# Kernel tuning notes

Hardware: AMD Instinct MI355X
Metric: run time of the kernel (lower is better)

Reference implementation:

```python
import jax, jax.numpy as jnp
import numpy as np
from jax import lax

B, N, C_IN, C_OUT = 4, 8192, 64, 128
STRIDE, RADIUS, K, L = 4, 0.1, 32, 2
EPS = 1e-5
M = N // STRIDE


def _bn(x, g, b):
    # training-mode batch norm, channel-first layout (B, C, ...)
    axes = (0,) + tuple(range(2, x.ndim))
    mean = jnp.mean(x, axis=axes, keepdims=True)
    var = jnp.mean((x - mean) ** 2, axis=axes, keepdims=True)
    sh = (1, -1) + (1,) * (x.ndim - 2)
    return (x - mean) * lax.rsqrt(var + EPS) * g.reshape(sh) + b.reshape(sh)


def _fps(points, m):
    # farthest point sampling starting at index 0 (matches fps_cuda semantics)
    b, n, _ = points.shape
    bi = jnp.arange(b)

    def body(carry, _):
        dis, last = carry
        lp = points[bi, last]  # (b,3)
        d = jnp.sum((points - lp[:, None, :]) ** 2, -1)
        dis = jnp.minimum(dis, d)
        return (dis, jnp.argmax(dis, -1).astype(jnp.int32)), last

    init = (jnp.full((b, n), 1e10, points.dtype), jnp.zeros((b,), jnp.int32))
    _, idx = lax.scan(body, init, None, length=m)
    return idx.T  # (b, m)


def _ball_query(radius, k, centroids, points, features):
    # first k points within radius of each centroid; pad with first hit
    b, n, _ = points.shape
    d2 = jnp.sum((centroids[:, :, None, :] - points[:, None, :, :]) ** 2, -1)  # (b,m,n)
    key = jnp.where(d2 < radius * radius, jnp.arange(n, dtype=jnp.int32), n)
    neg, _ = lax.top_k(-key, k)  # k smallest keys = first k in-ball indices
    sel = -neg  # (b,m,k)
    sel = jnp.where(sel == n, sel[..., :1], sel)
    sel = jnp.clip(sel, 0, n - 1)
    bi = jnp.arange(b)[:, None, None]
    gp = jnp.transpose(points[bi, sel], (0, 3, 2, 1))  # (b,3,k,m)
    gf = None
    if features is not None:
        gf = jnp.transpose(features[bi, sel], (0, 3, 2, 1))  # (b,c,k,m)
    return gp, gf


def _forward(pos, x, p):
    b, n, _ = pos.shape
    m = n // STRIDE
    bi = jnp.arange(b)[:, None]
    fps_idx = _fps(pos, m)
    centroids = pos[bi, fps_idx]  # (b,m,3)
    # x_mlp: 1x1 conv + BN + ReLU
    f = jax.nn.relu(_bn(jnp.einsum('bnc,oc->bon', x, p['W_x']), p['g_x'], p['b_x']))
    feats = jnp.transpose(f, (0, 2, 1))  # (b,n,C_OUT)
    gp, gf = _ball_query(RADIUS, K, centroids, pos, feats)
    cT = jnp.transpose(centroids, (0, 2, 1))[:, :, None, :]  # (b,3,1,m)
    gp = (gp - cT) / RADIUS
    gp = jax.nn.relu(_bn(jnp.einsum('bckm,oc->bokm', gp, p['W_ps']), p['g_ps'], p['b_ps']))
    xf = jnp.transpose(jnp.max(gf + gp, axis=2), (0, 2, 1))  # (b,m,C_OUT)
    # gen_pe on downsampled points
    R2 = RADIUS * 2
    gpe, _ = _ball_query(R2, K, centroids, centroids, None)
    gpe = (gpe - cT) / R2
    pe = jax.nn.relu(_bn(jnp.einsum('bckm,oc->bokm', gpe, p['W_pe']), p['g_pe'], p['b_pe']))
    # InvResMLP blocks
    for i in range(L):
        xc = jnp.transpose(xf, (0, 2, 1))  # (b,C,m)
        xc = jax.nn.relu(_bn(jnp.einsum('bcm,oc->bom', xc, p['W1'][i]), p['g1'][i], p['b1'][i]))
        feats_i = jnp.transpose(xc, (0, 2, 1))  # (b,m,C)
        _, gfi = _ball_query(R2, K, centroids, centroids, feats_i)
        g = jnp.max(gfi + pe, axis=2)  # (b,C,m)
        g = jax.nn.relu(_bn(jnp.einsum('bcm,oc->bom', g, p['W2a'][i]), p['g2a'][i], p['b2a'][i]))
        g = _bn(jnp.einsum('bcm,oc->bom', g, p['W2b'][i]), p['g2b'][i], p['b2b'][i])
        xf = jax.nn.relu(feats_i + jnp.transpose(g, (0, 2, 1)))
    return centroids, xf


def setup_inputs() -> dict:
    key = jax.random.key(0)
    ks = jax.random.split(key, 12)
    d = {
        'pos': jax.random.uniform(ks[0], (B, N, 3), jnp.float32),
        'x': jax.random.normal(ks[1], (B, N, C_IN), jnp.float32),
        'W_x': jax.random.normal(ks[2], (C_OUT, C_IN), jnp.float32) * 0.05,
        'g_x': jnp.ones((C_OUT,), jnp.float32), 'b_x': jnp.zeros((C_OUT,), jnp.float32),
        'W_ps': jax.random.normal(ks[3], (C_OUT, 3), jnp.float32) * 0.1,
        'g_ps': jnp.ones((C_OUT,), jnp.float32), 'b_ps': jnp.zeros((C_OUT,), jnp.float32),
        'W_pe': jax.random.normal(ks[4], (C_OUT, 3), jnp.float32) * 0.1,
        'g_pe': jnp.ones((C_OUT,), jnp.float32), 'b_pe': jnp.zeros((C_OUT,), jnp.float32),
        'W1': jax.random.normal(ks[5], (L, C_OUT, C_OUT), jnp.float32) * 0.05,
        'g1': jnp.ones((L, C_OUT), jnp.float32), 'b1': jnp.zeros((L, C_OUT), jnp.float32),
        'W2a': jax.random.normal(ks[6], (L, C_OUT, C_OUT), jnp.float32) * 0.05,
        'g2a': jnp.ones((L, C_OUT), jnp.float32), 'b2a': jnp.zeros((L, C_OUT), jnp.float32),
        'W2b': jax.random.normal(ks[7], (L, C_OUT, C_OUT), jnp.float32) * 0.05,
        'g2b': jnp.ones((L, C_OUT), jnp.float32), 'b2b': jnp.zeros((L, C_OUT), jnp.float32),
    }
    return d


def reference(pos, x, W_x, g_x, b_x, W_ps, g_ps, b_ps, W_pe, g_pe, b_pe,
              W1, g1, b1, W2a, g2a, b2a, W2b, g2b, b2b):
    p = dict(W_x=W_x, g_x=g_x, b_x=b_x, W_ps=W_ps, g_ps=g_ps, b_ps=b_ps,
             W_pe=W_pe, g_pe=g_pe, b_pe=b_pe, W1=W1, g1=g1, b1=b1,
             W2a=W2a, g2a=g2a, b2a=b2a, W2b=W2b, g2b=g2b, b2b=b2b)
    return _forward(pos, x, p)
```

## Files before the change

kernel.cpp:

```cpp
#include <hip/hip_runtime.h>


#define BB 4
#define NN 8192
#define MM 2048
#define KK 32
#define CI 64
#define CO 128
#define SG 16

typedef float vf2 __attribute__((ext_vector_type(2)));

#define ST_X 0
#define MO_PS 256
#define MO_PE 272
#define ST1 288
#define ST2A 800
#define ST2B (800 + 2 * SG * 256)
#define ST_TOTAL (ST2B + 512)

__device__ __forceinline__ float sq3(float dx, float dy, float dz) {
#pragma clang fp contract(off)
  return dx * dx + dy * dy + dz * dz;
}

__device__ __forceinline__ void fin_stats_d(const double* st, float gam,
                                            float bet, double cnt, int ch,
                                            float* sc, float* sh) {
  double mean = st[ch] / cnt;
  double var = st[128 + ch] / cnt - mean * mean;
  if (var < 0) var = 0;
  double s = (double)gam / sqrt(var + 1e-5);
  *sc = (float)s;
  *sh = (float)((double)bet - mean * s);
}

__device__ __forceinline__ void fin_mom_d(const double* mo, const float* Wrow,
                                          float gam, float bet, double cnt,
                                          float* sc, float* sh) {
  double w0 = Wrow[0], w1 = Wrow[1], w2 = Wrow[2];
  double mx = mo[0] / cnt, my = mo[1] / cnt, mz = mo[2] / cnt;
  double sxx = mo[3] / cnt, sxy = mo[4] / cnt, sxz = mo[5] / cnt;
  double syy = mo[6] / cnt, syz = mo[7] / cnt, szz = mo[8] / cnt;
  double mean = w0 * mx + w1 * my + w2 * mz;
  double ey2 = w0 * w0 * sxx + w1 * w1 * syy + w2 * w2 * szz +
               2.0 * (w0 * w1 * sxy + w0 * w2 * sxz + w1 * w2 * syz);
  double var = ey2 - mean * mean;
  if (var < 0) var = 0;
  double s = (double)gam / sqrt(var + 1e-5);
  *sc = (float)s;
  *sh = (float)((double)bet - mean * s);
}

__global__ void k_zero(double* s) {
  int i = blockIdx.x * 256 + threadIdx.x;
  if (i < ST_TOTAL) s[i] = 0.0;
}

template <int CTRL>
__device__ __forceinline__ int dpp_i(int v) {
  return __builtin_amdgcn_update_dpp(v, v, CTRL, 0xF, 0xF, false);
}
template <int CTRL>
__device__ __forceinline__ float dpp_f(float v) {
  return __int_as_float(dpp_i<CTRL>(__float_as_int(v)));
}

#define FT 512
#define NP 8
#define NW 8

__global__ __launch_bounds__(FT) void k_fps_conv(
    const float* __restrict__ pos, const float* __restrict__ x,
    const float* __restrict__ W_x, float* __restrict__ cent,
    float* __restrict__ fpre, double* __restrict__ stats) {
  __shared__ alignas(16) float s_wv[NW];
  __shared__ alignas(16) int s_wi[NW];
  __shared__ alignas(16) float s_pts[NN * 3];
  int t = threadIdx.x;
  if (blockIdx.x >= BB) {
    int cb = blockIdx.x - BB;
    int o = t & 127, q = t >> 7;
    float4 w[CI / 4];
    const float4* Wv = (const float4*)(W_x + (size_t)o * CI);
#pragma unroll
    for (int i = 0; i < CI / 4; i++) w[i] = Wv[i];
    int row0 = cb * 128;
    float ssum = 0.f, ssq = 0.f;
    for (int r = 0; r < 128; r += 4) {
      int row = __builtin_amdgcn_readfirstlane(row0 + r + q);
      const float* xr = x + (size_t)row * CI;
      float acc = 0.f;
#pragma unroll
      for (int i = 0; i < CI / 4; i++) {
        float4 a = *(const float4*)(xr + 4 * i);
        acc += a.x * w[i].x + a.y * w[i].y + a.z * w[i].z + a.w * w[i].w;
      }
      fpre[(size_t)row * CO + o] = acc;
      ssum += acc;
      ssq += acc * acc;
    }
    atomicAdd(&stats[ST_X + o], (double)ssum);
    atomicAdd(&stats[ST_X + 128 + o], (double)ssq);
    return;
  }
  int b = blockIdx.x;
  const float* P = pos + (size_t)b * NN * 3;
  float* C = cent + (size_t)b * MM * 3;
  int lane = t & 63, w = t >> 6;
  for (int i = t; i < (NN * 3) / 4; i += FT) {
    ((float4*)s_pts)[i] = ((const float4*)P)[i];
  }
  vf2 px[NP], py[NP], pz[NP], ds[NP];
#pragma unroll
  for (int s = 0; s < NP; s++) {
    int ia = (2 * s) * FT + t;
    int ib = ia + FT;
    px[s] = (vf2){P[ia * 3 + 0], P[ib * 3 + 0]};
    py[s] = (vf2){P[ia * 3 + 1], P[ib * 3 + 1]};
    pz[s] = (vf2){P[ia * 3 + 2], P[ib * 3 + 2]};
    ds[s] = (vf2){1e10f, 1e10f};
  }
  float lx = P[0], ly = P[1], lz = P[2];
  if (t == 0) {
    C[0] = lx;
    C[1] = ly;
    C[2] = lz;
  }
  __syncthreads();
  for (int m = 1; m < MM; m++) {
    vf2 l2x = (vf2){lx, lx}, l2y = (vf2){ly, ly}, l2z = (vf2){lz, lz};
    vf2 bmax = (vf2){-1.0f, -1.0f};
    {
#pragma clang fp contract(off)
#pragma unroll
      for (int s = 0; s < NP; s++) {
        vf2 dx = px[s] - l2x;
        vf2 dy = py[s] - l2y;
        vf2 dz = pz[s] - l2z;
        vf2 d2 = dx * dx + dy * dy + dz * dz;
        vf2 nd = __builtin_elementwise_min(ds[s], d2);
        ds[s] = nd;
        bmax = __builtin_elementwise_max(bmax, nd);
      }
    }
    float bv = fmaxf(bmax.x, bmax.y);
    bv = fmaxf(bv, dpp_f<0x111>(bv));
    bv = fmaxf(bv, dpp_f<0x112>(bv));
    bv = fmaxf(bv, dpp_f<0x114>(bv));
    bv = fmaxf(bv, dpp_f<0x118>(bv));
    bv = fmaxf(bv, dpp_f<0x142>(bv));
    bv = fmaxf(bv, dpp_f<0x143>(bv));
    if (lane == 63) s_wv[w] = bv;
    float gw63 =
        __int_as_float(__builtin_amdgcn_readlane(__float_as_int(bv), 63));
    __syncthreads();
    float4 va = ((const float4*)s_wv)[0];
    float4 vb = ((const float4*)s_wv)[1];
    float gmax = fmaxf(fmaxf(fmaxf(va.x, va.y), fmaxf(va.z, va.w)),
                       fmaxf(fmaxf(vb.x, vb.y), fmaxf(vb.z, vb.w)));
    int bi = 0x7fffffff;
    if (gw63 == gmax) {
#pragma unroll
      for (int s = 0; s < NP; s++) {
        int ia = (2 * s) * FT + t;
        int ib2 = ia + FT;
        bi = (ds[s].x == gmax) ? (ia < bi ? ia : bi) : bi;
        bi = (ds[s].y == gmax) ? (ib2 < bi ? ib2 : bi) : bi;
      }
      int u;
      u = dpp_i<0x111>(bi); bi = u < bi ? u : bi;
      u = dpp_i<0x112>(bi); bi = u < bi ? u : bi;
      u = dpp_i<0x114>(bi); bi = u < bi ? u : bi;
      u = dpp_i<0x118>(bi); bi = u < bi ? u : bi;
      u = dpp_i<0x142>(bi); bi = u < bi ? u : bi;
      u = dpp_i<0x143>(bi); bi = u < bi ? u : bi;
    }
    if (lane == 63) s_wi[w] = bi;
    __syncthreads();
    int4 ia4 = ((const int4*)s_wi)[0];
    int4 ib4 = ((const int4*)s_wi)[1];
    int g0 = ia4.x < ia4.y ? ia4.x : ia4.y;
    int g1 = ia4.z < ia4.w ? ia4.z : ia4.w;
    int g2 = ib4.x < ib4.y ? ib4.x : ib4.y;
    int g3 = ib4.z < ib4.w ? ib4.z : ib4.w;
    g0 = g0 < g1 ? g0 : g1;
    g2 = g2 < g3 ? g2 : g3;
    int gidx = g0 < g2 ? g0 : g2;
    lx = s_pts[gidx * 3 + 0];
    ly = s_pts[gidx * 3 + 1];
    lz = s_pts[gidx * 3 + 2];
    if (t == 0) {
      C[m * 3 + 0] = lx;
      C[m * 3 + 1] = ly;
      C[m * 3 + 2] = lz;
    }
  }
}

__global__ __launch_bounds__(256) void k_bq2(const float* __restrict__ pos,
                                             const float* __restrict__ cent,
                                             int* __restrict__ sel1,
                                             int* __restrict__ sel2,
                                             double* __restrict__ stats) {
  int lane = threadIdx.x & 63, w = threadIdx.x >> 6;
  const float* pts;
  int npts, pair;
  float rsq, inv_r;
  int* sel;
  double* mom;
  int half = (BB * MM) / 4;
  if (blockIdx.x < half) {
    pts = pos; npts = NN; rsq = 0.01f; inv_r = 10.0f;
    sel = sel1; mom = stats + MO_PS;
    pair = blockIdx.x * 4 + w;
  } else {
    pts = cent; npts = MM; rsq = 0.04f; inv_r = 5.0f;
    sel = sel2; mom = stats + MO_PE;
    pair = (blockIdx.x - half) * 4 + w;
  }
  int b = pair / MM;
  const float* P = pts + (size_t)b * npts * 3;
  const float* C = cent + (size_t)pair * 3;
  float cx = C[0], cy = C[1], cz = C[2];
  __shared__ int s_sel[4][KK];
  __shared__ float s_mom[4][9];
  int cnt = 0;
  int nch = npts >> 6;
  for (int ch = 0; ch < nch; ch++) {
    int i = (ch << 6) + lane;
    float d2 = sq3(P[i * 3 + 0] - cx, P[i * 3 + 1] - cy, P[i * 3 + 2] - cz);
    bool hit = d2 < rsq;
    unsigned long long mk = __ballot(hit);
    if (mk) {
      int pre = __popcll(mk & ((1ull << lane) - 1ull));
      int k = cnt + pre;
      if (hit && k < KK) s_sel[w][k] = i;
      cnt += __popcll(mk);
      if (cnt >= KK) break;
    }
  }
  int total = cnt < KK ? cnt : KK;
  int myidx = 0;
  if (lane < KK) {
    int v = (lane < total) ? s_sel[w][lane] : s_sel[w][0];
    sel[(size_t)pair * KK + lane] = v;
    myidx = v;
  }
  float gx = 0.f, gy = 0.f, gz = 0.f;
  if (lane < KK) {
    gx = (P[myidx * 3 + 0] - cx) * inv_r;
    gy = (P[myidx * 3 + 1] - cy) * inv_r;
    gz = (P[myidx * 3 + 2] - cz) * inv_r;
  }
  float v9[9] = {gx, gy, gz, gx * gx, gx * gy, gx * gz, gy * gy, gy * gz, gz * gz};
#pragma unroll
  for (int j = 0; j < 9; j++) {
#pragma unroll
    for (int off = 32; off > 0; off >>= 1) v9[j] += __shfl_xor(v9[j], off);
  }
  if (lane == 0) {
#pragma unroll
    for (int j = 0; j < 9; j++) s_mom[w][j] = v9[j];
  }
  __syncthreads();
  if (threadIdx.x < 9) {
    double a = (double)s_mom[0][threadIdx.x] + s_mom[1][threadIdx.x] +
               s_mom[2][threadIdx.x] + s_mom[3][threadIdx.x];
    atomicAdd(&mom[threadIdx.x], a);
  }
}

__global__ __launch_bounds__(128) void k_xf(
    const float* __restrict__ pos, const float* __restrict__ cent,
    const int* __restrict__ sel1, const float* __restrict__ fpre,
    const float* __restrict__ Wps, const float* __restrict__ g_ps,
    const float* __restrict__ b_ps, const float* __restrict__ g_x,
    const float* __restrict__ b_x, const double* __restrict__ stats,
    float* __restrict__ xf) {
  int pair = blockIdx.x;
  int b = pair >> 11;
  int o = threadIdx.x;
  float sx, hx, sp, hp;
  fin_stats_d(stats + ST_X, g_x[o], b_x[o], (double)(BB * NN), o, &sx, &hx);
  fin_mom_d(stats + MO_PS, Wps + o * 3, g_ps[o], b_ps[o],
            (double)(BB * MM * KK), &sp, &hp);
  float w0 = Wps[o * 3 + 0], w1 = Wps[o * 3 + 1], w2 = Wps[o * 3 + 2];
  const float* C = cent + (size_t)pair * 3;
  float cx = C[0], cy = C[1], cz = C[2];
  const float* P = pos + (size_t)b * NN * 3;
  const float* F = fpre + (size_t)b * NN * CO;
  __shared__ int s_idx[KK];
  if (o < KK) s_idx[o] = sel1[(size_t)pair * KK + o];
  __syncthreads();
  float acc = -1e30f;
#pragma unroll 4
  for (int k = 0; k < KK; k++) {
    int idx = __builtin_amdgcn_readfirstlane(s_idx[k]);
    float gx = (P[idx * 3 + 0] - cx) * 10.0f;
    float gy = (P[idx * 3 + 1] - cy) * 10.0f;
    float gz = (P[idx * 3 + 2] - cz) * 10.0f;
    float y = fmaxf((w0 * gx + w1 * gy + w2 * gz) * sp + hp, 0.f);
    float f = fmaxf(F[(size_t)idx * CO + o] * sx + hx, 0.f);
    float v = y + f;
    acc = v > acc ? v : acc;
  }
  xf[(size_t)pair * CO + o] = acc;
}

__global__ __launch_bounds__(256) void k_conv_plain(
    const float* __restrict__ in, const float* __restrict__ W,
    float* __restrict__ out, double* __restrict__ stats, int rows_per_block) {
  int o = threadIdx.x & 127, half = threadIdx.x >> 7;
  float4 w[CO / 4];
  const float4* Wv = (const float4*)(W + (size_t)o * CO);
#pragma unroll
  for (int i = 0; i < CO / 4; i++) w[i] = Wv[i];
  int row0 = blockIdx.x * rows_per_block;
  float ssum = 0.f, ssq = 0.f;
  for (int r = 0; r < rows_per_block; r += 2) {
    int row = __builtin_amdgcn_readfirstlane(row0 + r + half);
    const float* xr = in + (size_t)row * CO;
    float acc = 0.f;
#pragma unroll
    for (int i = 0; i < CO / 4; i++) {
      float4 a = *(const float4*)(xr + 4 * i);
      acc += a.x * w[i].x + a.y * w[i].y + a.z * w[i].z + a.w * w[i].w;
    }
    out[(size_t)row * CO + o] = acc;
    ssum += acc;
    ssq += acc * acc;
  }
  atomicAdd(&stats[o], (double)ssum);
  atomicAdd(&stats[128 + o], (double)ssq);
}

__global__ __launch_bounds__(256) void k_conv_bnin(
    const float* __restrict__ in, const float* __restrict__ W,
    const double* __restrict__ st_grp, const float* __restrict__ gam,
    const float* __restrict__ bet, float* __restrict__ out,
    double* __restrict__ stats, int rows_per_block) {
  __shared__ float s_sc[128], s_sh[128];
  int t = threadIdx.x;
  if (t < 128) {
    double sum = 0, ssq2 = 0;
#pragma unroll
    for (int g = 0; g < SG; g++) {
      sum += st_grp[g * 256 + t];
      ssq2 += st_grp[g * 256 + 128 + t];
    }
    double cnt = (double)(BB * MM);
    double mean = sum / cnt;
    double var = ssq2 / cnt - mean * mean;
    if (var < 0) var = 0;
    double s = (double)gam[t] / sqrt(var + 1e-5);
    s_sc[t] = (float)s;
    s_sh[t] = (float)((double)bet[t] - mean * s);
  }
  __syncthreads();
  int o = t & 127, half = t >> 7;
  float4 w[CO / 4];
  const float4* Wv = (const float4*)(W + (size_t)o * CO);
#pragma unroll
  for (int i = 0; i < CO / 4; i++) w[i] = Wv[i];
  int row0 = blockIdx.x * rows_per_block;
  float ssum = 0.f, ssq = 0.f;
  for (int r = 0; r < rows_per_block; r += 2) {
    int row = __builtin_amdgcn_readfirstlane(row0 + r + half);
    const float* xr = in + (size_t)row * CO;
    float acc = 0.f;
#pragma unroll
    for (int i = 0; i < CO / 4; i++) {
      float4 a = *(const float4*)(xr + 4 * i);
      a.x = fmaxf(a.x * s_sc[4 * i + 0] + s_sh[4 * i + 0], 0.f);
      a.y = fmaxf(a.y * s_sc[4 * i + 1] + s_sh[4 * i + 1], 0.f);
      a.z = fmaxf(a.z * s_sc[4 * i + 2] + s_sh[4 * i + 2], 0.f);
      a.w = fmaxf(a.w * s_sc[4 * i + 3] + s_sh[4 * i + 3], 0.f);
      acc += a.x * w[i].x + a.y * w[i].y + a.z * w[i].z + a.w * w[i].w;
    }
    out[(size_t)row * CO + o] = acc;
    ssum += acc;
    ssq += acc * acc;
  }
  atomicAdd(&stats[o], (double)ssum);
  atomicAdd(&stats[128 + o], (double)ssq);
}

__global__ __launch_bounds__(256) void k_conv_resid(
    const float* __restrict__ y1prev, const float* __restrict__ y2bprev,
    const double* __restrict__ st1p, const float* __restrict__ g1p,
    const float* __restrict__ b1p, const double* __restrict__ st2bp,
    const float* __restrict__ g2bp, const float* __restrict__ b2bp,
    const float* __restrict__ W, float* __restrict__ y1out,
    double* __restrict__ stats, int rows_per_block) {
  __shared__ float s_s1[128], s_h1[128], s_s2[128], s_h2[128];
  int t = threadIdx.x;
  if (t < 128) {
    fin_stats_d(st1p, g1p[t], b1p[t], (double)(BB * MM), t, &s_s1[t], &s_h1[t]);
    fin_stats_d(st2bp, g2bp[t], b2bp[t], (double)(BB * MM), t, &s_s2[t],
                &s_h2[t]);
  }
  __syncthreads();
  int o = t & 127, half = t >> 7;
  float4 w[CO / 4];
  const float4* Wv = (const float4*)(W + (size_t)o * CO);
#pragma unroll
  for (int i = 0; i < CO / 4; i++) w[i] = Wv[i];
  int row0 = blockIdx.x * rows_per_block;
  float ssum = 0.f, ssq = 0.f;
  for (int r = 0; r < rows_per_block; r += 2) {
    int row = __builtin_amdgcn_readfirstlane(row0 + r + half);
    const float* ar = y1prev + (size_t)row * CO;
    const float* br = y2bprev + (size_t)row * CO;
    float acc = 0.f;
#pragma unroll
    for (int i = 0; i < CO / 4; i++) {
      float4 a = *(const float4*)(ar + 4 * i);
      float4 bb = *(const float4*)(br + 4 * i);
      float x0 = fmaxf(fmaxf(a.x * s_s1[4 * i + 0] + s_h1[4 * i + 0], 0.f) +
                           (bb.x * s_s2[4 * i + 0] + s_h2[4 * i + 0]), 0.f);
      float x1 = fmaxf(fmaxf(a.y * s_s1[4 * i + 1] + s_h1[4 * i + 1], 0.f) +
                           (bb.y * s_s2[4 * i + 1] + s_h2[4 * i + 1]), 0.f);
      float x2 = fmaxf(fmaxf(a.z * s_s1[4 * i + 2] + s_h1[4 * i + 2], 0.f) +
                           (bb.z * s_s2[4 * i + 2] + s_h2[4 * i + 2]), 0.f);
      float x3 = fmaxf(fmaxf(a.w * s_s1[4 * i + 3] + s_h1[4 * i + 3], 0.f) +
                           (bb.w * s_s2[4 * i + 3] + s_h2[4 * i + 3]), 0.f);
      acc += x0 * w[i].x + x1 * w[i].y + x2 * w[i].z + x3 * w[i].w;
    }
    y1out[(size_t)row * CO + o] = acc;
    ssum += acc;
    ssq += acc * acc;
  }
  atomicAdd(&stats[o], (double)ssum);
  atomicAdd(&stats[128 + o], (double)ssq);
}

__global__ __launch_bounds__(128) void k_gconv(
    const float* __restrict__ cent, const int* __restrict__ sel2,
    const float* __restrict__ y1in, const double* __restrict__ st1,
    const float* __restrict__ g1v, const float* __restrict__ b1v,
    const double* __restrict__ mo_pe, const float* __restrict__ Wpe,
    const float* __restrict__ gpe, const float* __restrict__ bpe,
    const float* __restrict__ W2a, float* __restrict__ y2a,
    double* __restrict__ st2a) {
  int pair = blockIdx.x;
  int b = pair >> 11;
  int o = threadIdx.x;
  float s1, h1, se, he;
  fin_stats_d(st1, g1v[o], b1v[o], (double)(BB * MM), o, &s1, &h1);
  fin_mom_d(mo_pe, Wpe + o * 3, gpe[o], bpe[o], (double)(BB * MM * KK), &se,
            &he);
  float w0 = Wpe[o * 3 + 0], w1 = Wpe[o * 3 + 1], w2 = Wpe[o * 3 + 2];
  const float* C = cent + (size_t)pair * 3;
  float cx = C[0], cy = C[1], cz = C[2];
  const float* CB = cent + (size_t)b * MM * 3;
  const float* Y = y1in + (size_t)b * MM * CO;
  __shared__ int s_idx[KK];
  __shared__ float s_g[128];
  if (o < KK) s_idx[o] = sel2[(size_t)pair * KK + o];
  __syncthreads();
  float acc = -1e30f;
#pragma unroll 4
  for (int k = 0; k < KK; k++) {
    int idx = __builtin_amdgcn_readfirstlane(s_idx[k]);
    float gx = (CB[idx * 3 + 0] - cx) * 5.0f;
    float gy = (CB[idx * 3 + 1] - cy) * 5.0f;
    float gz = (CB[idx * 3 + 2] - cz) * 5.0f;
    float pe = fmaxf((w0 * gx + w1 * gy + w2 * gz) * se + he, 0.f);
    float f = fmaxf(Y[(size_t)idx * CO + o] * s1 + h1, 0.f);
    float v = pe + f;
    acc = v > acc ? v : acc;
  }
  s_g[o] = acc;
  __syncthreads();
  const float4* Wv = (const float4*)(W2a + (size_t)o * CO);
  const float4* gv = (const float4*)s_g;
  float dot = 0.f;
#pragma unroll
  for (int i = 0; i < CO / 4; i++) {
    float4 a = gv[i];
    float4 ww = Wv[i];
    dot += a.x * ww.x + a.y * ww.y + a.z * ww.z + a.w * ww.w;
  }
  y2a[(size_t)pair * CO + o] = dot;
  int grp = pair & (SG - 1);
  atomicAdd(&st2a[grp * 256 + o], (double)dot);
  atomicAdd(&st2a[grp * 256 + 128 + o], (double)(dot * dot));
}

__global__ __launch_bounds__(256) void k_resid_fin(
    const float* __restrict__ y1b, const double* __restrict__ st1,
    const float* __restrict__ g1v, const float* __restrict__ b1v,
    const float* __restrict__ y2b, const double* __restrict__ st2b,
    const float* __restrict__ g2bv, const float* __restrict__ b2bv,
    float* __restrict__ xf) {
  int i = blockIdx.x * 256 + threadIdx.x;
  int o = i & 127;
  float s1, h1, s2, h2;
  fin_stats_d(st1, g1v[o], b1v[o], (double)(BB * MM), o, &s1, &h1);
  fin_stats_d(st2b, g2bv[o], b2bv[o], (double)(BB * MM), o, &s2, &h2);
  float f = fmaxf(y1b[i] * s1 + h1, 0.f);
  float v = y2b[i] * s2 + h2;
  xf[i] = fmaxf(f + v, 0.f);
}

extern "C" void kernel_launch(void* const* d_in, const int* in_sizes, int n_in,
                              void* d_out, int out_size, void* d_ws,
                              size_t ws_size, hipStream_t stream) {
  const float* pos = (const float*)d_in[0];
  const float* x = (const float*)d_in[1];
  const float* W_x = (const float*)d_in[2];
  const float* g_x = (const float*)d_in[3];
  const float* b_x = (const float*)d_in[4];
  const float* W_ps = (const float*)d_in[5];
  const float* g_ps = (const float*)d_in[6];
  const float* b_ps = (const float*)d_in[7];
  const float* W_pe = (const float*)d_in[8];
  const float* g_pe = (const float*)d_in[9];
  const float* b_pe = (const float*)d_in[10];
  const float* W1 = (const float*)d_in[11];
  const float* g1 = (const float*)d_in[12];
  const float* b1 = (const float*)d_in[13];
  const float* W2a = (const float*)d_in[14];
  const float* g2a = (const float*)d_in[15];
  const float* b2a = (const float*)d_in[16];
  const float* W2b = (const float*)d_in[17];
  const float* g2b = (const float*)d_in[18];
  const float* b2b = (const float*)d_in[19];

  float* cent = (float*)d_out;
  float* xf = cent + (size_t)BB * MM * 3;

  char* p = (char*)d_ws;
  double* stats = (double*)p; p += (size_t)ST_TOTAL * sizeof(double);
  int* sel1 = (int*)p;        p += (size_t)BB * MM * KK * sizeof(int);
  int* sel2 = (int*)p;        p += (size_t)BB * MM * KK * sizeof(int);
  float* fpre = (float*)p;    p += (size_t)BB * NN * CO * sizeof(float);
  float* y1a = (float*)p;     p += (size_t)BB * MM * CO * sizeof(float);
  float* y1b = (float*)p;     p += (size_t)BB * MM * CO * sizeof(float);
  float* y2a = (float*)p;     p += (size_t)BB * MM * CO * sizeof(float);
  float* y2b = (float*)p;     p += (size_t)BB * MM * CO * sizeof(float);

  k_zero<<<(ST_TOTAL + 255) / 256, 256, 0, stream>>>(stats);
  k_fps_conv<<<BB + 256, FT, 0, stream>>>(pos, x, W_x, cent, fpre, stats);
  k_bq2<<<(BB * MM) / 2, 256, 0, stream>>>(pos, cent, sel1, sel2, stats);
  k_xf<<<BB * MM, 128, 0, stream>>>(pos, cent, sel1, fpre, W_ps, g_ps, b_ps,
                                    g_x, b_x, stats, xf);
  k_conv_plain<<<128, 256, 0, stream>>>(xf, W1, y1a, stats + ST1, 64);
  k_gconv<<<BB * MM, 128, 0, stream>>>(cent, sel2, y1a, stats + ST1, g1, b1,
                                       stats + MO_PE, W_pe, g_pe, b_pe, W2a,
                                       y2a, stats + ST2A);
  k_conv_bnin<<<128, 256, 0, stream>>>(y2a, W2b, stats + ST2A, g2a, b2a, y2b,
                                       stats + ST2B, 64);
  k_conv_resid<<<128, 256, 0, stream>>>(
      y1a, y2b, stats + ST1, g1, b1, stats + ST2B, g2b, b2b, W1 + CO * CO, y1b,
      stats + ST1 + 256, 64);
  k_gconv<<<BB * MM, 128, 0, stream>>>(cent, sel2, y1b, stats + ST1 + 256,
                                       g1 + 128, b1 + 128, stats + MO_PE, W_pe,
                                       g_pe, b_pe, W2a + CO * CO, y2a,
                                       stats + ST2A + SG * 256);
  k_conv_bnin<<<128, 256, 0, stream>>>(y2a, W2b + CO * CO,
                                       stats + ST2A + SG * 256, g2a + 128,
                                       b2a + 128, y2b, stats + ST2B + 256, 64);
  k_resid_fin<<<(BB * MM * CO) / 256, 256, 0, stream>>>(
      y1b, stats + ST1 + 256, g1 + 128, b1 + 128, y2b, stats + ST2B + 256,
      g2b + 128, b2b + 128, xf);
}
```

Baseline: 2.687 ms.

## Fuse neighbor max-pool with first conv, group BN stats, unroll ball query

The neighbor max-pool kernel now also computes the first 128x128 conv per centroid from shared memory, which removes the separate k_conv_plain launch and the xf round trip. Its per-channel BN statistics are spread across SG grouped slots to cut atomic contention, and consumers sum the groups through a new fin_grp_d helper. The ball-query scan handles four 64-point chunks per iteration to expose more memory-level parallelism, at the cost of possibly scanning past the early-exit point. The zeroing kernel is replaced by hipMemsetAsync. The fused kernel issues one double atomic pair per block per channel (8192 blocks), which may itself create atomic traffic.

```diff
diff --git a/kernel.cpp b/kernel.cpp
--- a/kernel.cpp
+++ b/kernel.cpp
@@ -15,8 +15,8 @@
 #define MO_PS 256
 #define MO_PE 272
 #define ST1 288
-#define ST2A 800
-#define ST2B (800 + 2 * SG * 256)
+#define ST2A (288 + 2 * SG * 256)
+#define ST2B (ST2A + 2 * SG * 256)
 #define ST_TOTAL (ST2B + 512)
 
 __device__ __forceinline__ float sq3(float dx, float dy, float dz) {
@@ -29,6 +29,23 @@
                                             float* sc, float* sh) {
   double mean = st[ch] / cnt;
   double var = st[128 + ch] / cnt - mean * mean;
+  if (var < 0) var = 0;
+  double s = (double)gam / sqrt(var + 1e-5);
+  *sc = (float)s;
+  *sh = (float)((double)bet - mean * s);
+}
+
+__device__ __forceinline__ void fin_grp_d(const double* st, float gam,
+                                          float bet, double cnt, int ch,
+                                          float* sc, float* sh) {
+  double sum = 0, ssq = 0;
+#pragma unroll
+  for (int g = 0; g < SG; g++) {
+    sum += st[g * 256 + ch];
+    ssq += st[g * 256 + 128 + ch];
+  }
+  double mean = sum / cnt;
+  double var = ssq / cnt - mean * mean;
   if (var < 0) var = 0;
   double s = (double)gam / sqrt(var + 1e-5);
   *sc = (float)s;
@@ -50,11 +67,6 @@
   double s = (double)gam / sqrt(var + 1e-5);
   *sc = (float)s;
   *sh = (float)((double)bet - mean * s);
-}
-
-__global__ void k_zero(double* s) {
-  int i = blockIdx.x * 256 + threadIdx.x;
-  if (i < ST_TOTAL) s[i] = 0.0;
 }
 
 template <int CTRL>
@@ -226,19 +238,49 @@
   __shared__ int s_sel[4][KK];
   __shared__ float s_mom[4][9];
   int cnt = 0;
-  int nch = npts >> 6;
-  for (int ch = 0; ch < nch; ch++) {
-    int i = (ch << 6) + lane;
-    float d2 = sq3(P[i * 3 + 0] - cx, P[i * 3 + 1] - cy, P[i * 3 + 2] - cz);
-    bool hit = d2 < rsq;
-    unsigned long long mk = __ballot(hit);
-    if (mk) {
-      int pre = __popcll(mk & ((1ull << lane) - 1ull));
-      int k = cnt + pre;
-      if (hit && k < KK) s_sel[w][k] = i;
-      cnt += __popcll(mk);
-      if (cnt >= KK) break;
-    }
+  unsigned long long ltm = (1ull << lane) - 1ull;
+  int nit = npts >> 8;
+  for (int ch = 0; ch < nit; ch++) {
+    int i0 = (ch << 8) + lane;
+    bool h0, h1, h2, h3;
+    {
+      float a0 = P[i0 * 3 + 0], a1 = P[i0 * 3 + 1], a2 = P[i0 * 3 + 2];
+      float b0 = P[(i0 + 64) * 3 + 0], b1 = P[(i0 + 64) * 3 + 1],
+            b2 = P[(i0 + 64) * 3 + 2];
+      float c0 = P[(i0 + 128) * 3 + 0], c1 = P[(i0 + 128) * 3 + 1],
+            c2 = P[(i0 + 128) * 3 + 2];
+      float e0 = P[(i0 + 192) * 3 + 0], e1 = P[(i0 + 192) * 3 + 1],
+            e2 = P[(i0 + 192) * 3 + 2];
+      h0 = sq3(a0 - cx, a1 - cy, a2 - cz) < rsq;
+      h1 = sq3(b0 - cx, b1 - cy, b2 - cz) < rsq;
+      h2 = sq3(c0 - cx, c1 - cy, c2 - cz) < rsq;
+      h3 = sq3(e0 - cx, e1 - cy, e2 - cz) < rsq;
+    }
+    unsigned long long m0 = __ballot(h0);
+    unsigned long long m1 = __ballot(h1);
+    unsigned long long m2 = __ballot(h2);
+    unsigned long long m3 = __ballot(h3);
+    if (m0) {
+      int k = cnt + __popcll(m0 & ltm);
+      if (h0 && k < KK) s_sel[w][k] = i0;
+      cnt += __popcll(m0);
+    }
+    if (m1) {
+      int k = cnt + __popcll(m1 & ltm);
+      if (h1 && k < KK) s_sel[w][k] = i0 + 64;
+      cnt += __popcll(m1);
+    }
+    if (m2) {
+      int k = cnt + __popcll(m2 & ltm);
+      if (h2 && k < KK) s_sel[w][k] = i0 + 128;
+      cnt += __popcll(m2);
+    }
+    if (m3) {
+      int k = cnt + __popcll(m3 & ltm);
+      if (h3 && k < KK) s_sel[w][k] = i0 + 192;
+      cnt += __popcll(m3);
+    }
+    if (cnt >= KK) break;
   }
   int total = cnt < KK ? cnt : KK;
   int myidx = 0;
@@ -271,13 +313,14 @@
   }
 }
 
-__global__ __launch_bounds__(128) void k_xf(
+__global__ __launch_bounds__(128) void k_xf_conv1(
     const float* __restrict__ pos, const float* __restrict__ cent,
     const int* __restrict__ sel1, const float* __restrict__ fpre,
     const float* __restrict__ Wps, const float* __restrict__ g_ps,
     const float* __restrict__ b_ps, const float* __restrict__ g_x,
     const float* __restrict__ b_x, const double* __restrict__ stats,
-    float* __restrict__ xf) {
+    const float* __restrict__ W1, float* __restrict__ y1a,
+    double* __restrict__ st1out) {
   int pair = blockIdx.x;
   int b = pair >> 11;
   int o = threadIdx.x;
@@ -291,6 +334,7 @@
   const float* P = pos + (size_t)b * NN * 3;
   const float* F = fpre + (size_t)b * NN * CO;
   __shared__ int s_idx[KK];
+  __shared__ float s_xf[128];
   if (o < KK) s_idx[o] = sel1[(size_t)pair * KK + o];
   __syncthreads();
   float acc = -1e30f;
@@ -305,34 +349,21 @@
     float v = y + f;
     acc = v > acc ? v : acc;
   }
-  xf[(size_t)pair * CO + o] = acc;
-}
-
-__global__ __launch_bounds__(256) void k_conv_plain(
-    const float* __restrict__ in, const float* __restrict__ W,
-    float* __restrict__ out, double* __restrict__ stats, int rows_per_block) {
-  int o = threadIdx.x & 127, half = threadIdx.x >> 7;
-  float4 w[CO / 4];
-  const float4* Wv = (const float4*)(W + (size_t)o * CO);
-#pragma unroll
-  for (int i = 0; i < CO / 4; i++) w[i] = Wv[i];
-  int row0 = blockIdx.x * rows_per_block;
-  float ssum = 0.f, ssq = 0.f;
-  for (int r = 0; r < rows_per_block; r += 2) {
-    int row = __builtin_amdgcn_readfirstlane(row0 + r + half);
-    const float* xr = in + (size_t)row * CO;
-    float acc = 0.f;
-#pragma unroll
-    for (int i = 0; i < CO / 4; i++) {
-      float4 a = *(const float4*)(xr + 4 * i);
-      acc += a.x * w[i].x + a.y * w[i].y + a.z * w[i].z + a.w * w[i].w;
-    }
-    out[(size_t)row * CO + o] = acc;
-    ssum += acc;
-    ssq += acc * acc;
-  }
-  atomicAdd(&stats[o], (double)ssum);
-  atomicAdd(&stats[128 + o], (double)ssq);
+  s_xf[o] = acc;
+  __syncthreads();
+  const float4* Wv = (const float4*)(W1 + (size_t)o * CO);
+  const float4* gv = (const float4*)s_xf;
+  float dot = 0.f;
+#pragma unroll
+  for (int i = 0; i < CO / 4; i++) {
+    float4 a = gv[i];
+    float4 ww = Wv[i];
+    dot += a.x * ww.x + a.y * ww.y + a.z * ww.z + a.w * ww.w;
+  }
+  y1a[(size_t)pair * CO + o] = dot;
+  int grp = pair & (SG - 1);
+  atomicAdd(&st1out[grp * 256 + o], (double)dot);
+  atomicAdd(&st1out[grp * 256 + 128 + o], (double)(dot * dot));
 }
 
 __global__ __launch_bounds__(256) void k_conv_bnin(
@@ -343,19 +374,8 @@
   __shared__ float s_sc[128], s_sh[128];
   int t = threadIdx.x;
   if (t < 128) {
-    double sum = 0, ssq2 = 0;
-#pragma unroll
-    for (int g = 0; g < SG; g++) {
-      sum += st_grp[g * 256 + t];
-      ssq2 += st_grp[g * 256 + 128 + t];
-    }
-    double cnt = (double)(BB * MM);
-    double mean = sum / cnt;
-    double var = ssq2 / cnt - mean * mean;
-    if (var < 0) var = 0;
-    double s = (double)gam[t] / sqrt(var + 1e-5);
-    s_sc[t] = (float)s;
-    s_sh[t] = (float)((double)bet[t] - mean * s);
+    fin_grp_d(st_grp, gam[t], bet[t], (double)(BB * MM), t, &s_sc[t],
+              &s_sh[t]);
   }
   __syncthreads();
   int o = t & 127, half = t >> 7;
@@ -396,7 +416,7 @@
   __shared__ float s_s1[128], s_h1[128], s_s2[128], s_h2[128];
   int t = threadIdx.x;
   if (t < 128) {
-    fin_stats_d(st1p, g1p[t], b1p[t], (double)(BB * MM), t, &s_s1[t], &s_h1[t]);
+    fin_grp_d(st1p, g1p[t], b1p[t], (double)(BB * MM), t, &s_s1[t], &s_h1[t]);
     fin_stats_d(st2bp, g2bp[t], b2bp[t], (double)(BB * MM), t, &s_s2[t],
                 &s_h2[t]);
   }
@@ -431,8 +451,9 @@
     ssum += acc;
     ssq += acc * acc;
   }
-  atomicAdd(&stats[o], (double)ssum);
-  atomicAdd(&stats[128 + o], (double)ssq);
+  int grp = blockIdx.x & (SG - 1);
+  atomicAdd(&stats[grp * 256 + o], (double)ssum);
+  atomicAdd(&stats[grp * 256 + 128 + o], (double)ssq);
 }
 
 __global__ __launch_bounds__(128) void k_gconv(
@@ -447,7 +468,7 @@
   int b = pair >> 11;
   int o = threadIdx.x;
   float s1, h1, se, he;
-  fin_stats_d(st1, g1v[o], b1v[o], (double)(BB * MM), o, &s1, &h1);
+  fin_grp_d(st1, g1v[o], b1v[o], (double)(BB * MM), o, &s1, &h1);
   fin_mom_d(mo_pe, Wpe + o * 3, gpe[o], bpe[o], (double)(BB * MM * KK), &se,
             &he);
   float w0 = Wpe[o * 3 + 0], w1 = Wpe[o * 3 + 1], w2 = Wpe[o * 3 + 2];
@@ -497,7 +518,7 @@
   int i = blockIdx.x * 256 + threadIdx.x;
   int o = i & 127;
   float s1, h1, s2, h2;
-  fin_stats_d(st1, g1v[o], b1v[o], (double)(BB * MM), o, &s1, &h1);
+  fin_grp_d(st1, g1v[o], b1v[o], (double)(BB * MM), o, &s1, &h1);
   fin_stats_d(st2b, g2bv[o], b2bv[o], (double)(BB * MM), o, &s2, &h2);
   float f = fmaxf(y1b[i] * s1 + h1, 0.f);
   float v = y2b[i] * s2 + h2;
@@ -541,12 +562,12 @@
   float* y2a = (float*)p;     p += (size_t)BB * MM * CO * sizeof(float);
   float* y2b = (float*)p;     p += (size_t)BB * MM * CO * sizeof(float);
 
-  k_zero<<<(ST_TOTAL + 255) / 256, 256, 0, stream>>>(stats);
+  hipMemsetAsync(stats, 0, (size_t)ST_TOTAL * sizeof(double), stream);
   k_fps_conv<<<BB + 256, FT, 0, stream>>>(pos, x, W_x, cent, fpre, stats);
   k_bq2<<<(BB * MM) / 2, 256, 0, stream>>>(pos, cent, sel1, sel2, stats);
-  k_xf<<<BB * MM, 128, 0, stream>>>(pos, cent, sel1, fpre, W_ps, g_ps, b_ps,
-                                    g_x, b_x, stats, xf);
-  k_conv_plain<<<128, 256, 0, stream>>>(xf, W1, y1a, stats + ST1, 64);
+  k_xf_conv1<<<BB * MM, 128, 0, stream>>>(pos, cent, sel1, fpre, W_ps, g_ps,
+                                          b_ps, g_x, b_x, stats, W1, y1a,
+                                          stats + ST1);
   k_gconv<<<BB * MM, 128, 0, stream>>>(cent, sel2, y1a, stats + ST1, g1, b1,
                                        stats + MO_PE, W_pe, g_pe, b_pe, W2a,
                                        y2a, stats + ST2A);
@@ -554,8 +575,8 @@
                                        stats + ST2B, 64);
   k_conv_resid<<<128, 256, 0, stream>>>(
       y1a, y2b, stats + ST1, g1, b1, stats + ST2B, g2b, b2b, W1 + CO * CO, y1b,
-      stats + ST1 + 256, 64);
-  k_gconv<<<BB * MM, 128, 0, stream>>>(cent, sel2, y1b, stats + ST1 + 256,
+      stats + ST1 + SG * 256, 64);
+  k_gconv<<<BB * MM, 128, 0, stream>>>(cent, sel2, y1b, stats + ST1 + SG * 256,
                                        g1 + 128, b1 + 128, stats + MO_PE, W_pe,
                                        g_pe, b_pe, W2a + CO * CO, y2a,
                                        stats + ST2A + SG * 256);
@@ -563,6 +584,6 @@
                                        stats + ST2A + SG * 256, g2a + 128,
                                        b2a + 128, y2b, stats + ST2B + 256, 64);
   k_resid_fin<<<(BB * MM * CO) / 256, 256, 0, stream>>>(
-      y1b, stats + ST1 + 256, g1 + 128, b1 + 128, y2b, stats + ST2B + 256,
-      g2b + 128, b2b + 128, xf);
-}
+      y1b, stats + ST1 + SG * 256, g1 + 128, b1 + 128, y2b,
+      stats + ST2B + 256, g2b + 128, b2b + 128, xf);
+}
```

New measurement: 2.679 ms. About the same (-0.3%).
